# Kernel optimization log

Measured on AMD Instinct MI355X. Metric: run time of the kernel, lower is better.

## Reference

```python
import jax, jax.numpy as jnp
import numpy as np

B, L, D = 4, 16384, 128          # batch, voxels per sample, d_model
DI, DS, DTR, K = 256, 16, 8, 4   # d_inner, d_state, dt_rank, conv kernel
N = B * L
EPS = 1e-5


def setup_inputs() -> dict:
    key = jax.random.key(0)
    ks = jax.random.split(key, 12)
    s = 0.02
    feats = jax.random.normal(ks[0], (N, D), jnp.float32)
    coords_xyz = jax.random.randint(ks[1], (N, 3), 0, 1024, jnp.int32)
    # per-batch Morton permutation + its inverse
    perm = jnp.stack([jax.random.permutation(jax.random.fold_in(ks[2], i), L) for i in range(B)]).astype(jnp.int32)
    inv_perm = jnp.argsort(perm, axis=1).astype(jnp.int32)
    return {
        'feats': feats,
        'pos_w': jax.random.normal(ks[3], (3, D), jnp.float32) * s,
        'pos_b': jnp.zeros((D,), jnp.float32),
        'rms_w': jnp.ones((D,), jnp.float32),
        'in_proj_w': jax.random.normal(ks[4], (D, 2 * DI), jnp.float32) * s,
        'conv_w': jax.random.normal(ks[5], (DI, K), jnp.float32) * s,
        'conv_b': jnp.zeros((DI,), jnp.float32),
        'x_proj_w': jax.random.normal(ks[6], (DI, DTR + 2 * DS), jnp.float32) * s,
        'dt_proj_w': jax.random.normal(ks[7], (DTR, DI), jnp.float32) * s,
        'dt_proj_b': jax.random.normal(ks[8], (DI,), jnp.float32) * 0.1,
        'A_log': jnp.log(jnp.broadcast_to(jnp.arange(1.0, DS + 1.0, dtype=jnp.float32), (DI, DS))),
        'D_param': jnp.ones((DI,), jnp.float32),
        'out_proj_w': jax.random.normal(ks[9], (DI, D), jnp.float32) * s,
        'ln_w': jnp.ones((D,), jnp.float32),
        'ln_b': jnp.zeros((D,), jnp.float32),
        'coords_xyz': coords_xyz,
        'perm': perm,
        'inv_perm': inv_perm,
    }


def _gssm(feats, pos_w, pos_b, rms_w, in_proj_w, conv_w, conv_b, x_proj_w,
          dt_proj_w, dt_proj_b, A_log, D_param, out_proj_w, ln_w, ln_b,
          coords_xyz, perm, inv_perm):
    # positional embedding of voxel coords
    pe = coords_xyz.astype(jnp.float32) @ pos_w + pos_b            # [N, D]
    h = (feats + pe).reshape(B, L, D)
    # gather into Morton order (per-batch fancy index)
    hm = jnp.take_along_axis(h, perm[:, :, None].astype(jnp.int32), axis=1)  # [B, L, D]
    # Mamba block: RMSNorm then mixer (block returns mixer output only)
    x = hm * jax.lax.rsqrt(jnp.mean(hm * hm, axis=-1, keepdims=True) + EPS) * rms_w
    xz = x @ in_proj_w                                             # [B, L, 2*DI]
    xi, z = xz[..., :DI], xz[..., DI:]
    # depthwise causal conv1d, kernel K
    xp = jnp.pad(xi, ((0, 0), (K - 1, 0), (0, 0)))
    xc = conv_b + sum(xp[:, j:j + L, :] * conv_w[:, j] for j in range(K))
    xc = jax.nn.silu(xc)                                           # [B, L, DI]
    dbc = xc @ x_proj_w                                            # [B, L, DTR+2*DS]
    dt, Bm, Cm = dbc[..., :DTR], dbc[..., DTR:DTR + DS], dbc[..., DTR + DS:]
    dt = jax.nn.softplus(dt @ dt_proj_w + dt_proj_b)               # [B, L, DI]
    A = -jnp.exp(A_log)                                            # [DI, DS]

    def step(hst, inp):
        x_t, dt_t, b_t, c_t = inp                                  # [B,DI],[B,DI],[B,DS],[B,DS]
        hst = jnp.exp(dt_t[..., None] * A) * hst + (dt_t * x_t)[..., None] * b_t[:, None, :]
        return hst, jnp.einsum('bds,bs->bd', hst, c_t)

    h0 = jnp.zeros((B, DI, DS), xc.dtype)
    _, ys = jax.lax.scan(step, h0, (xc.transpose(1, 0, 2), dt.transpose(1, 0, 2),
                                    Bm.transpose(1, 0, 2), Cm.transpose(1, 0, 2)))
    y = ys.transpose(1, 0, 2) + xc * D_param                       # [B, L, DI]
    y = y * jax.nn.silu(z)
    out = y @ out_proj_w                                           # [B, L, D]
    # scatter back to original voxel order
    out = jnp.take_along_axis(out, inv_perm[:, :, None].astype(jnp.int32), axis=1).reshape(N, D)
    # post-SSM LayerNorm
    mu = jnp.mean(out, axis=-1, keepdims=True)
    var = jnp.mean((out - mu) ** 2, axis=-1, keepdims=True)
    return (out - mu) * jax.lax.rsqrt(var + EPS) * ln_w + ln_b


def reference(feats, pos_w, pos_b, rms_w, in_proj_w, conv_w, conv_b, x_proj_w,
              dt_proj_w, dt_proj_b, A_log, D_param, out_proj_w, ln_w, ln_b,
              coords_xyz, perm, inv_perm):
    return _gssm(feats, pos_w, pos_b, rms_w, in_proj_w, conv_w, conv_b, x_proj_w,
                 dt_proj_w, dt_proj_b, A_log, D_param, out_proj_w, ln_w, ln_b,
                 coords_xyz, perm, inv_perm)
```

## Files before the change

kernel.cpp:

```cpp
#include <hip/hip_runtime.h>
#include <hip/hip_bf16.h>
#include <math.h>

#define B_   4
#define L_   16384
#define D_   128
#define DI_  256
#define DS_  16
#define DTR_ 8
#define N_   65536
#define NC_  128
#define LC_  128
#define TW_  16
#define TP_  260
#define EPS_ 1e-5f

typedef __hip_bfloat16 bf16;
typedef __attribute__((ext_vector_type(8))) short short8;
typedef __attribute__((ext_vector_type(4))) float f32x4;

__device__ __forceinline__ bool probe_bf16(const void* Dp) {
  return ((const unsigned*)Dp)[0] == 0x3F803F80u;
}
__device__ __forceinline__ float ldin(const void* p, size_t i, bool isb) {
  return isb ? __bfloat162float(((const bf16*)p)[i]) : ((const float*)p)[i];
}
__device__ __forceinline__ float4 ld4(const void* p, size_t i4, bool isb) {
  if (!isb) return ((const float4*)p)[i4];
  const ushort4 v = ((const ushort4*)p)[i4];
  float4 r;
  r.x = __uint_as_float((unsigned)v.x << 16);
  r.y = __uint_as_float((unsigned)v.y << 16);
  r.z = __uint_as_float((unsigned)v.z << 16);
  r.w = __uint_as_float((unsigned)v.w << 16);
  return r;
}
__device__ __forceinline__ void splitbf(float v, ushort& hi, ushort& lo) {
  bf16 h = __float2bfloat16(v);
  float rem = v - __bfloat162float(h);
  bf16 l = __float2bfloat16(rem);
  hi = *(ushort*)&h;
  lo = *(ushort*)&l;
}


__global__ __launch_bounds__(256) void k_xnorm(
    const void* __restrict__ feats, const void* __restrict__ pos_w,
    const void* __restrict__ pos_b, const void* __restrict__ rms_w,
    const int* __restrict__ coords, const int* __restrict__ perm,
    const void* __restrict__ Dprobe,
    ushort* __restrict__ xh, ushort* __restrict__ xl) {
  const bool isb = probe_bf16(Dprobe);
  int wv = threadIdx.x >> 6, lane = threadIdx.x & 63;
  int p = blockIdx.x * 4 + wv;
  int b = p >> 14;
  int srow = b * L_ + perm[p];
  float cx = (float)coords[srow*3+0];
  float cy = (float)coords[srow*3+1];
  float cz = (float)coords[srow*3+2];
  int i0 = lane, i1 = lane + 64;
  float h0 = ldin(feats,(size_t)srow*D_ + i0,isb) + cx*ldin(pos_w,i0,isb) + cy*ldin(pos_w,D_+i0,isb)
           + cz*ldin(pos_w,2*D_+i0,isb) + ldin(pos_b,i0,isb);
  float h1 = ldin(feats,(size_t)srow*D_ + i1,isb) + cx*ldin(pos_w,i1,isb) + cy*ldin(pos_w,D_+i1,isb)
           + cz*ldin(pos_w,2*D_+i1,isb) + ldin(pos_b,i1,isb);
  float ss = h0*h0 + h1*h1;
  #pragma unroll
  for (int off = 32; off; off >>= 1) ss += __shfl_xor(ss, off);
  float r = 1.0f / sqrtf(ss * (1.f/128.f) + EPS_);
  float v0 = h0 * r * ldin(rms_w,i0,isb);
  float v1 = h1 * r * ldin(rms_w,i1,isb);
  ushort a, bq;
  splitbf(v0, a, bq);
  xh[(size_t)p*D_ + i0] = a; xl[(size_t)p*D_ + i0] = bq;
  splitbf(v1, a, bq);
  xh[(size_t)p*D_ + i1] = a; xl[(size_t)p*D_ + i1] = bq;
}

__global__ __launch_bounds__(256) void k_prepw(
    const void* __restrict__ Win, const void* __restrict__ Dprobe,
    ushort* __restrict__ wth, ushort* __restrict__ wtl) {
  const bool isb = probe_bf16(Dprobe);
  int idx = blockIdx.x * 256 + threadIdx.x;
  int k = idx >> 9, n = idx & 511;
  float v = ldin(Win, (size_t)k*512 + n, isb);
  ushort a, b;
  splitbf(v, a, b);
  wth[(size_t)n*128 + k] = a;
  wtl[(size_t)n*128 + k] = b;
}

__global__ __launch_bounds__(256) void k_prepxw(
    const void* __restrict__ xW, const void* __restrict__ Dprobe,
    ushort* __restrict__ wxh, ushort* __restrict__ wxl) {
  const bool isb = probe_bf16(Dprobe);
  int idx = blockIdx.x * 256 + threadIdx.x;
  int q = idx >> 8, c = idx & 255;
  float v = (q < 40) ? ldin(xW, (size_t)c*40 + q, isb) : 0.f;
  ushort a, b;
  splitbf(v, a, b);
  wxh[idx] = a;
  wxl[idx] = b;
}

__global__ __launch_bounds__(256) void k_prepdtw(
    const void* __restrict__ dtW, const void* __restrict__ Dprobe,
    ushort* __restrict__ dtwh, ushort* __restrict__ dtwl) {
  const bool isb = probe_bf16(Dprobe);
  int idx = blockIdx.x * 256 + threadIdx.x;
  int d = idx >> 5, k = idx & 31;
  float v = (k < 8) ? ldin(dtW, (size_t)k*256 + d, isb) : 0.f;
  ushort a, b;
  splitbf(v, a, b);
  dtwh[idx] = a;
  dtwl[idx] = b;
}

__global__ __launch_bounds__(256) void k_inproj(
    const ushort* __restrict__ xh, const ushort* __restrict__ xl,
    const ushort* __restrict__ wth, const ushort* __restrict__ wtl,
    float* __restrict__ xiT, float* __restrict__ zB) {
  __shared__ short Ah[64*136];
  __shared__ short Al[64*136];
  __shared__ short Bh[32*136];
  __shared__ short Bl[32*136];
  int tid = threadIdx.x;
  int T0 = blockIdx.x * 64;
  int lane = tid & 63, w = tid >> 6;
  {
    int k0 = (tid & 15) * 8;
    int m0 = tid >> 4;
    #pragma unroll
    for (int mi = 0; mi < 4; ++mi) {
      int m = m0 + 16*mi;
      *(short8*)&Ah[m*136 + k0] = *(const short8*)&xh[(size_t)(T0+m)*128 + k0];
      *(short8*)&Al[m*136 + k0] = *(const short8*)&xl[(size_t)(T0+m)*128 + k0];
    }
  }
  __syncthreads();
  int mloc = lane & 15, quad = lane >> 4;
  short8 afh[4], afl[4];
  #pragma unroll
  for (int ks = 0; ks < 4; ++ks) {
    int ka = ks*32 + quad*8;
    afh[ks] = *(const short8*)&Ah[(w*16 + mloc)*136 + ka];
    afl[ks] = *(const short8*)&Al[(w*16 + mloc)*136 + ka];
  }
  for (int ct = 0; ct < 16; ++ct) {
    int C0 = ct * 32;
    __syncthreads();
    {
      int k0 = (tid & 15) * 8;
      int n0 = tid >> 4;
      #pragma unroll
      for (int ni = 0; ni < 2; ++ni) {
        int n = n0 + 16*ni;
        *(short8*)&Bh[n*136 + k0] = *(const short8*)&wth[(size_t)(C0+n)*128 + k0];
        *(short8*)&Bl[n*136 + k0] = *(const short8*)&wtl[(size_t)(C0+n)*128 + k0];
      }
    }
    __syncthreads();
    #pragma unroll
    for (int nt = 0; nt < 2; ++nt) {
      f32x4 acc = {0.f, 0.f, 0.f, 0.f};
      #pragma unroll
      for (int ks = 0; ks < 4; ++ks) {
        int kb = ks*32 + quad*8;
        short8 bh = *(const short8*)&Bh[(nt*16 + mloc)*136 + kb];
        short8 bl = *(const short8*)&Bl[(nt*16 + mloc)*136 + kb];
        acc = __builtin_amdgcn_mfma_f32_16x16x32_bf16(afh[ks], bh, acc, 0, 0, 0);
        acc = __builtin_amdgcn_mfma_f32_16x16x32_bf16(afl[ks], bh, acc, 0, 0, 0);
        acc = __builtin_amdgcn_mfma_f32_16x16x32_bf16(afh[ks], bl, acc, 0, 0, 0);
      }
      int col = C0 + nt*16 + mloc;
      int trow = T0 + w*16 + quad*4;
      if (col < 256) {
        *(float4*)&xiT[(size_t)col*N_ + trow] = make_float4(acc[0], acc[1], acc[2], acc[3]);
      } else {
        int zc = col - 256;
        #pragma unroll
        for (int r = 0; r < 4; ++r)
          zB[(size_t)(trow + r)*256 + zc] = acc[r];
      }
    }
  }
}

__global__ __launch_bounds__(256) void k_conv_s(
    const float* __restrict__ xiT, const void* __restrict__ conv_w,
    const void* __restrict__ conv_b, const void* __restrict__ Dprobe,
    float* __restrict__ xcT) {
  const bool isb = probe_bf16(Dprobe);
  int idx = blockIdx.x * 256 + threadIdx.x;
  int c = idx >> 16;
  int t = idx & 65535;
  int l = t & (L_-1);
  const float* row = xiT + (size_t)c * N_;
  float acc = ldin(conv_b, c, isb);
  if (l >= 3) acc += row[t-3] * ldin(conv_w, c*4+0, isb);
  if (l >= 2) acc += row[t-2] * ldin(conv_w, c*4+1, isb);
  if (l >= 1) acc += row[t-1] * ldin(conv_w, c*4+2, isb);
  acc += row[t] * ldin(conv_w, c*4+3, isb);
  xcT[(size_t)c*N_ + t] = acc / (1.f + __expf(-acc));
}

__global__ __launch_bounds__(256) void k_xproj(
    const float* __restrict__ xcT,
    const ushort* __restrict__ wxh, const ushort* __restrict__ wxl,
    const ushort* __restrict__ dtwh, const ushort* __restrict__ dtwl,
    const void* __restrict__ dtb, const void* __restrict__ Dprobe,
    float* __restrict__ dtT, float* __restrict__ BmB, float* __restrict__ CmB) {
  const bool isb = probe_bf16(Dprobe);
  __shared__ float s40[64*52];
  __shared__ float sdtb[256];
  const int tid = threadIdx.x;
  const int lane = tid & 63, w = tid >> 6;
  const int T0 = blockIdx.x * 64;
  const int n15 = lane & 15, quad = lane >> 4;
  sdtb[tid] = ldin(dtb, tid, isb);

  f32x4 acc0 = {0.f,0.f,0.f,0.f}, acc1 = {0.f,0.f,0.f,0.f}, acc2 = {0.f,0.f,0.f,0.f};
  const float* xb = &xcT[(size_t)(quad*8)*N_ + T0 + w*16 + n15];
  #pragma unroll
  for (int ks = 0; ks < 8; ++ks) {
    short8 bh, bl;
    #pragma unroll
    for (int j = 0; j < 8; ++j) {
      ushort h, l;
      splitbf(xb[(size_t)(ks*32 + j)*N_], h, l);
      bh[j] = (short)h; bl[j] = (short)l;
    }
    #pragma unroll
    for (int mt = 0; mt < 3; ++mt) {
      const size_t aoff = (size_t)(mt*16 + n15)*256 + ks*32 + quad*8;
      short8 ah = *(const short8*)&wxh[aoff];
      short8 al = *(const short8*)&wxl[aoff];
      f32x4 a = (mt==0) ? acc0 : (mt==1) ? acc1 : acc2;
      a = __builtin_amdgcn_mfma_f32_16x16x32_bf16(ah, bh, a, 0, 0, 0);
      a = __builtin_amdgcn_mfma_f32_16x16x32_bf16(al, bh, a, 0, 0, 0);
      a = __builtin_amdgcn_mfma_f32_16x16x32_bf16(ah, bl, a, 0, 0, 0);
      if (mt==0) acc0 = a; else if (mt==1) acc1 = a; else acc2 = a;
    }
  }
  {
    const int trow = (w*16 + n15)*52;
    #pragma unroll
    for (int r = 0; r < 4; ++r) {
      s40[trow +      quad*4 + r] = acc0[r];
      s40[trow + 16 + quad*4 + r] = acc1[r];
      s40[trow + 32 + quad*4 + r] = acc2[r];
    }
  }
  __syncthreads();
  {
    int t = tid >> 2, fq = tid & 3;
    float4 bm = *(const float4*)&s40[t*52 + 8  + fq*4];
    float4 cm = *(const float4*)&s40[t*52 + 24 + fq*4];
    *(float4*)&BmB[(size_t)(T0+t)*16 + fq*4] = bm;
    *(float4*)&CmB[(size_t)(T0+t)*16 + fq*4] = cm;
  }
  short8 dh, dl;
  #pragma unroll
  for (int j = 0; j < 8; ++j) {
    ushort h, l;
    splitbf(s40[(w*16 + n15)*52 + quad*8 + j], h, l);
    dh[j] = (short)h; dl[j] = (short)l;
  }
  #pragma unroll
  for (int mt = 0; mt < 16; ++mt) {
    f32x4 a = {0.f,0.f,0.f,0.f};
    const size_t doff = (size_t)(mt*16 + n15)*32 + quad*8;
    short8 ah = *(const short8*)&dtwh[doff];
    short8 al = *(const short8*)&dtwl[doff];
    a = __builtin_amdgcn_mfma_f32_16x16x32_bf16(ah, dh, a, 0, 0, 0);
    a = __builtin_amdgcn_mfma_f32_16x16x32_bf16(al, dh, a, 0, 0, 0);
    a = __builtin_amdgcn_mfma_f32_16x16x32_bf16(ah, dl, a, 0, 0, 0);
    #pragma unroll
    for (int r = 0; r < 4; ++r) {
      int d = mt*16 + quad*4 + r;
      float pre = a[r] + sdtb[d];
      float sp = (pre > 20.f) ? pre : log1pf(__expf(pre));
      dtT[(size_t)d*N_ + T0 + w*16 + n15] = sp;
    }
  }
}

__global__ __launch_bounds__(512, 4) void k_scan1(
    const float* __restrict__ dtT, const float* __restrict__ xcT,
    const float* __restrict__ BmB, const void* __restrict__ A_log,
    const void* __restrict__ Dprobe, float* __restrict__ Pb, float* __restrict__ Sb) {
  const bool isb = probe_bf16(Dprobe);
  __shared__ float sdt[TW_*TP_];
  __shared__ float sxc[TW_*TP_];
  __shared__ float sbm[LC_*16];
  const int tid = threadIdx.x;
  const int blk = blockIdx.x;
  const int b = blk >> 7, ch = blk & 127;
  const int T0 = b * L_ + ch * LC_;
  const int d = tid >> 1, sh = tid & 1, s0 = sh * 8;
  {
    int f = tid * 4;
    *(float4*)&sbm[f] = *(const float4*)&BmB[(size_t)T0*16 + f];
  }
  float Al[8];
  #pragma unroll
  for (int s = 0; s < 8; ++s) Al[s] = -__expf(ldin(A_log, d*16 + s0 + s, isb));
  const float Al0 = (sh == 0) ? Al[0] : -__expf(ldin(A_log, d*16, isb));
  bool fast = true;
  #pragma unroll
  for (int s = 0; s < 8; ++s)
    fast = fast && (fabsf(Al[s] - (Al[0] + (float)s * Al0)) <= 1e-4f * fabsf(Al[s]));
  float h[8];
  #pragma unroll
  for (int s = 0; s < 8; ++s) h[s] = 0.f;
  float sumdt = 0.f;
  float4 vd[2], vx[2];
  #pragma unroll
  for (int q = 0; q < 2; ++q) {
    int idx = q*512 + tid;
    int c2 = idx >> 2, i4 = (idx & 3) * 4;
    size_t off = (size_t)c2*N_ + T0 + i4;
    vd[q] = *(const float4*)&dtT[off];
    vx[q] = *(const float4*)&xcT[off];
  }
  for (int it = 0; it < LC_; it += TW_) {
    __syncthreads();
    #pragma unroll
    for (int q = 0; q < 2; ++q) {
      int idx = q*512 + tid;
      int c2 = idx >> 2, i4 = (idx & 3) * 4;
      sdt[(i4+0)*TP_ + c2] = vd[q].x; sdt[(i4+1)*TP_ + c2] = vd[q].y;
      sdt[(i4+2)*TP_ + c2] = vd[q].z; sdt[(i4+3)*TP_ + c2] = vd[q].w;
      sxc[(i4+0)*TP_ + c2] = vx[q].x; sxc[(i4+1)*TP_ + c2] = vx[q].y;
      sxc[(i4+2)*TP_ + c2] = vx[q].z; sxc[(i4+3)*TP_ + c2] = vx[q].w;
    }
    __syncthreads();
    if (it + TW_ < LC_) {
      #pragma unroll
      for (int q = 0; q < 2; ++q) {
        int idx = q*512 + tid;
        int c2 = idx >> 2, i4 = (idx & 3) * 4;
        size_t off = (size_t)c2*N_ + T0 + it + TW_ + i4;
        vd[q] = *(const float4*)&dtT[off];
        vx[q] = *(const float4*)&xcT[off];
      }
    }
    if (fast) {
      #pragma unroll
      for (int i = 0; i < TW_; ++i) {
        float dtv = sdt[i*TP_ + d];
        float xcv = sxc[i*TP_ + d];
        sumdt += dtv;
        float du = dtv * xcv;
        float e1 = __expf(dtv * Al0);
        float p  = __expf(dtv * Al[0]);
        const float4 b0 = *(const float4*)&sbm[(it+i)*16 + s0];
        const float4 b1 = *(const float4*)&sbm[(it+i)*16 + s0 + 4];
        h[0] = p*h[0] + du*b0.x; p *= e1;
        h[1] = p*h[1] + du*b0.y; p *= e1;
        h[2] = p*h[2] + du*b0.z; p *= e1;
        h[3] = p*h[3] + du*b0.w; p *= e1;
        h[4] = p*h[4] + du*b1.x; p *= e1;
        h[5] = p*h[5] + du*b1.y; p *= e1;
        h[6] = p*h[6] + du*b1.z; p *= e1;
        h[7] = p*h[7] + du*b1.w;
      }
    } else {
      #pragma unroll
      for (int i = 0; i < TW_; ++i) {
        float dtv = sdt[i*TP_ + d];
        float xcv = sxc[i*TP_ + d];
        sumdt += dtv;
        float du = dtv * xcv;
        const float* bmr = &sbm[(it+i)*16 + s0];
        #pragma unroll
        for (int s = 0; s < 8; ++s)
          h[s] = __expf(dtv * Al[s]) * h[s] + du * bmr[s];
      }
    }
  }
  size_t rec = ((size_t)blk*256 + d) * 16 + s0;
  #pragma unroll
  for (int s = 0; s < 8; ++s) {
    Sb[rec + s] = h[s];
    Pb[rec + s] = __expf(Al[s] * sumdt);
  }
}

__global__ __launch_bounds__(256) void k_scan2(
    const float* __restrict__ Pb, const float* __restrict__ Sb, float* __restrict__ Hin) {
  int tid = blockIdx.x * 256 + threadIdx.x;
  int b = tid >> 12, r = tid & 4095;
  float h = 0.f;
  for (int ch = 0; ch < NC_; ++ch) {
    size_t rec = ((size_t)(b*NC_ + ch)) * 4096 + r;
    Hin[rec] = h;
    h = Pb[rec] * h + Sb[rec];
  }
}

__global__ __launch_bounds__(512, 4) void k_scan3(
    const float* __restrict__ dtT, const float* __restrict__ xcT,
    const float* __restrict__ BmB, const float* __restrict__ CmB,
    const void* __restrict__ A_log, const void* __restrict__ Dp,
    const float* __restrict__ Hin, float* __restrict__ zyg) {
  const bool isb = probe_bf16(Dp);
  __shared__ float sdt[TW_*TP_];
  __shared__ float sxc[TW_*TP_];
  __shared__ float sbm[LC_*16];
  __shared__ float scm[LC_*16];
  const int tid = threadIdx.x;
  const int blk = blockIdx.x;
  const int b = blk >> 7, ch = blk & 127;
  const int T0 = b * L_ + ch * LC_;
  const int d = tid >> 1, sh = tid & 1, s0 = sh * 8;
  {
    int f = tid * 4;
    *(float4*)&sbm[f] = *(const float4*)&BmB[(size_t)T0*16 + f];
    *(float4*)&scm[f] = *(const float4*)&CmB[(size_t)T0*16 + f];
  }
  float Al[8];
  #pragma unroll
  for (int s = 0; s < 8; ++s) Al[s] = -__expf(ldin(A_log, d*16 + s0 + s, isb));
  const float Al0 = (sh == 0) ? Al[0] : -__expf(ldin(A_log, d*16, isb));
  bool fast = true;
  #pragma unroll
  for (int s = 0; s < 8; ++s)
    fast = fast && (fabsf(Al[s] - (Al[0] + (float)s * Al0)) <= 1e-4f * fabsf(Al[s]));
  float h[8];
  size_t rec = ((size_t)blk*256 + d) * 16 + s0;
  #pragma unroll
  for (int s = 0; s < 8; ++s) h[s] = Hin[rec + s];
  const float Dv = ldin(Dp, d, isb);
  float4 vd[2], vx[2];
  #pragma unroll
  for (int q = 0; q < 2; ++q) {
    int idx = q*512 + tid;
    int c2 = idx >> 2, i4 = (idx & 3) * 4;
    size_t off = (size_t)c2*N_ + T0 + i4;
    vd[q] = *(const float4*)&dtT[off];
    vx[q] = *(const float4*)&xcT[off];
  }
  for (int it = 0; it < LC_; it += TW_) {
    __syncthreads();
    #pragma unroll
    for (int q = 0; q < 2; ++q) {
      int idx = q*512 + tid;
      int c2 = idx >> 2, i4 = (idx & 3) * 4;
      sdt[(i4+0)*TP_ + c2] = vd[q].x; sdt[(i4+1)*TP_ + c2] = vd[q].y;
      sdt[(i4+2)*TP_ + c2] = vd[q].z; sdt[(i4+3)*TP_ + c2] = vd[q].w;
      sxc[(i4+0)*TP_ + c2] = vx[q].x; sxc[(i4+1)*TP_ + c2] = vx[q].y;
      sxc[(i4+2)*TP_ + c2] = vx[q].z; sxc[(i4+3)*TP_ + c2] = vx[q].w;
    }
    __syncthreads();
    if (it + TW_ < LC_) {
      #pragma unroll
      for (int q = 0; q < 2; ++q) {
        int idx = q*512 + tid;
        int c2 = idx >> 2, i4 = (idx & 3) * 4;
        size_t off = (size_t)c2*N_ + T0 + it + TW_ + i4;
        vd[q] = *(const float4*)&dtT[off];
        vx[q] = *(const float4*)&xcT[off];
      }
    }
    float zv[TW_];
    if (sh == 0) {
      #pragma unroll
      for (int i = 0; i < TW_; ++i) zv[i] = zyg[(size_t)(T0 + it + i)*256 + d];
    }
    #pragma unroll
    for (int i = 0; i < TW_; ++i) {
      float dtv = sdt[i*TP_ + d];
      float xcv = sxc[i*TP_ + d];
      float du = dtv * xcv;
      const float4 b0 = *(const float4*)&sbm[(it+i)*16 + s0];
      const float4 b1 = *(const float4*)&sbm[(it+i)*16 + s0 + 4];
      const float4 c0 = *(const float4*)&scm[(it+i)*16 + s0];
      const float4 c1 = *(const float4*)&scm[(it+i)*16 + s0 + 4];
      float yp = 0.f;
      if (fast) {
        float e1 = __expf(dtv * Al0);
        float p  = __expf(dtv * Al[0]);
        h[0] = p*h[0] + du*b0.x; yp += h[0]*c0.x; p *= e1;
        h[1] = p*h[1] + du*b0.y; yp += h[1]*c0.y; p *= e1;
        h[2] = p*h[2] + du*b0.z; yp += h[2]*c0.z; p *= e1;
        h[3] = p*h[3] + du*b0.w; yp += h[3]*c0.w; p *= e1;
        h[4] = p*h[4] + du*b1.x; yp += h[4]*c1.x; p *= e1;
        h[5] = p*h[5] + du*b1.y; yp += h[5]*c1.y; p *= e1;
        h[6] = p*h[6] + du*b1.z; yp += h[6]*c1.z; p *= e1;
        h[7] = p*h[7] + du*b1.w; yp += h[7]*c1.w;
      } else {
        const float* bmr = &sbm[(it+i)*16 + s0];
        const float* cmr = &scm[(it+i)*16 + s0];
        #pragma unroll
        for (int s = 0; s < 8; ++s) {
          h[s] = __expf(dtv * Al[s]) * h[s] + du * bmr[s];
          yp += h[s] * cmr[s];
        }
      }
      float yt = yp + __shfl_xor(yp, 1);
      if (sh == 0) {
        float yv = yt + xcv * Dv;
        float zvv = zv[i];
        float sil = zvv / (1.f + __expf(-zvv));
        zyg[(size_t)(T0 + it + i)*256 + d] = yv * sil;
      }
    }
  }
}

__global__ __launch_bounds__(256) void k_outproj(
    const float* __restrict__ yg, const void* __restrict__ W2,
    const void* __restrict__ Dprobe, float* __restrict__ outp) {
  const bool isb = probe_bf16(Dprobe);
  __shared__ float As[64*68];
  __shared__ float Bs[64*128];
  int tid = threadIdx.x;
  int T0 = blockIdx.x * 64;
  int tm = tid & 15, tn = tid >> 4;
  float acc[4][8] = {{0.f}};
  for (int kb = 0; kb < 256; kb += 64) {
    {
      int m = tid & 63, kq = tid >> 6;
      #pragma unroll
      for (int r = 0; r < 4; ++r) {
        int k0 = kq*16 + r*4;
        float4 v = *(const float4*)&yg[(size_t)(T0+m)*256 + kb + k0];
        As[(k0+0)*68+m] = v.x; As[(k0+1)*68+m] = v.y;
        As[(k0+2)*68+m] = v.z; As[(k0+3)*68+m] = v.w;
      }
      int n = (tid & 31)*4, kq2 = tid >> 5;
      #pragma unroll
      for (int p = 0; p < 8; ++p) {
        int k = kq2 + p*8;
        float4 w = ld4(W2, ((size_t)(kb+k)*128 + n) >> 2, isb);
        *(float4*)&Bs[k*128 + n] = w;
      }
    }
    __syncthreads();
    #pragma unroll 4
    for (int k = 0; k < 64; ++k) {
      float4 a  = *(const float4*)&As[k*68 + tm*4];
      float4 b0 = *(const float4*)&Bs[k*128 + tn*8];
      float4 b1 = *(const float4*)&Bs[k*128 + tn*8 + 4];
      float am[4] = {a.x, a.y, a.z, a.w};
      float bn[8] = {b0.x, b0.y, b0.z, b0.w, b1.x, b1.y, b1.z, b1.w};
      #pragma unroll
      for (int mi = 0; mi < 4; ++mi)
        #pragma unroll
        for (int ni = 0; ni < 8; ++ni)
          acc[mi][ni] += am[mi] * bn[ni];
    }
    __syncthreads();
  }
  #pragma unroll
  for (int mi = 0; mi < 4; ++mi) {
    size_t m = (size_t)(T0 + tm*4 + mi);
    *(float4*)&outp[m*128 + tn*8]     = make_float4(acc[mi][0], acc[mi][1], acc[mi][2], acc[mi][3]);
    *(float4*)&outp[m*128 + tn*8 + 4] = make_float4(acc[mi][4], acc[mi][5], acc[mi][6], acc[mi][7]);
  }
}

__global__ __launch_bounds__(256) void k_ln(
    const float* __restrict__ outp, const int* __restrict__ perm,
    const void* __restrict__ ln_w, const void* __restrict__ ln_b,
    const void* __restrict__ Dprobe, void* __restrict__ out) {
  const bool isb = probe_bf16(Dprobe);
  int wv = threadIdx.x >> 6, lane = threadIdx.x & 63;
  int p = blockIdx.x * 4 + wv;
  int b = p >> 14;
  int dest = b * L_ + perm[p];
  float v0 = outp[(size_t)p*128 + lane];
  float v1 = outp[(size_t)p*128 + lane + 64];
  float s1 = v0 + v1, s2 = v0*v0 + v1*v1;
  #pragma unroll
  for (int off = 32; off; off >>= 1) {
    s1 += __shfl_xor(s1, off);
    s2 += __shfl_xor(s2, off);
  }
  float mean = s1 * (1.f/128.f);
  float var  = s2 * (1.f/128.f) - mean*mean;
  float r = 1.0f / sqrtf(var + EPS_);
  float o0 = (v0 - mean)*r*ldin(ln_w,lane,isb)    + ldin(ln_b,lane,isb);
  float o1 = (v1 - mean)*r*ldin(ln_w,lane+64,isb) + ldin(ln_b,lane+64,isb);
  if (isb) {
    ((bf16*)out)[(size_t)dest*128 + lane]      = __float2bfloat16(o0);
    ((bf16*)out)[(size_t)dest*128 + lane + 64] = __float2bfloat16(o1);
  } else {
    ((float*)out)[(size_t)dest*128 + lane]      = o0;
    ((float*)out)[(size_t)dest*128 + lane + 64] = o1;
  }
}

extern "C" void kernel_launch(void* const* d_in, const int* in_sizes, int n_in,
                              void* d_out, int out_size, void* d_ws, size_t ws_size,
                              hipStream_t stream) {
  const void* feats    = d_in[0];
  const void* pos_w    = d_in[1];
  const void* pos_b    = d_in[2];
  const void* rms_w    = d_in[3];
  const void* in_proj  = d_in[4];
  const void* conv_w   = d_in[5];
  const void* conv_b   = d_in[6];
  const void* x_proj   = d_in[7];
  const void* dt_projw = d_in[8];
  const void* dt_projb = d_in[9];
  const void* A_log    = d_in[10];
  const void* D_param  = d_in[11];
  const void* out_proj = d_in[12];
  const void* ln_w     = d_in[13];
  const void* ln_b     = d_in[14];
  const int*  coords   = (const int*)d_in[15];
  const int*  perm     = (const int*)d_in[16];

  float* ws = (float*)d_ws;
  const size_t NN = (size_t)N_;
  ushort* xh  = (ushort*)ws;
  ushort* xl  = (ushort*)(ws + 64*NN);
  ushort* wth = (ushort*)(ws + 640*NN);
  ushort* wtl = (ushort*)(ws + 641*NN);
  ushort* wxh  = (ushort*)ws;
  ushort* wxl  = ((ushort*)ws) + 12288;
  ushort* dtwh = ((ushort*)ws) + 24576;
  ushort* dtwl = ((ushort*)ws) + 32768;
  float* Pb   = ws;
  float* Sb   = ws + 32*NN;
  float* Hin  = ws + 64*NN;
  float* BmB  = ws + 96*NN;
  float* CmB  = ws + 112*NN;
  float* xiT  = ws + 128*NN;
  float* dtT  = ws + 128*NN;
  float* outp = ws + 128*NN;
  float* zB   = ws + 384*NN;
  float* yg   = zB;
  float* xcT  = ws + 640*NN;

  k_prepw<<<256, 256, 0, stream>>>(in_proj, D_param, wth, wtl);
  k_xnorm<<<N_/4, 256, 0, stream>>>(feats, pos_w, pos_b, rms_w, coords, perm, D_param, xh, xl);
  k_inproj<<<N_/64, 256, 0, stream>>>(xh, xl, wth, wtl, xiT, zB);
  k_prepxw<<<48, 256, 0, stream>>>(x_proj, D_param, wxh, wxl);
  k_prepdtw<<<32, 256, 0, stream>>>(dt_projw, D_param, dtwh, dtwl);
  k_conv_s<<<(DI_*N_)/256, 256, 0, stream>>>(xiT, conv_w, conv_b, D_param, xcT);
  k_xproj<<<N_/64, 256, 0, stream>>>(xcT, wxh, wxl, dtwh, dtwl, dt_projb, D_param, dtT, BmB, CmB);
  k_scan1<<<B_*NC_, 512, 0, stream>>>(dtT, xcT, BmB, A_log, D_param, Pb, Sb);
  k_scan2<<<64, 256, 0, stream>>>(Pb, Sb, Hin);
  k_scan3<<<B_*NC_, 512, 0, stream>>>(dtT, xcT, BmB, CmB, A_log, D_param, Hin, zB);
  k_outproj<<<N_/64, 256, 0, stream>>>(yg, out_proj, D_param, outp);
  k_ln<<<N_/4, 256, 0, stream>>>(outp, perm, ln_w, ln_b, D_param, d_out);
}
```

Baseline: 543.0 us.

## Store z/y-gated buffer channel-major and give each scan thread all 16 states

The z half of in_proj is now written channel-major ([DI][N]) with float4 stores instead of scattered token-major stores. The scan3 kernel uses 256 threads per block, each owning one channel and all 16 states, so it no longer needs the lane-pair shuffle reduction. It reads and writes z/y as float4 along the token axis. out_proj now loads its A tile directly from the channel-major layout without an in-shared transpose. The trade is fewer threads per block and more registers per thread in the scan, which lowers parallelism inside the sequential recurrence.

```diff
diff --git a/kernel.cpp b/kernel.cpp
--- a/kernel.cpp
+++ b/kernel.cpp
@@ -118,7 +118,7 @@
 __global__ __launch_bounds__(256) void k_inproj(
     const ushort* __restrict__ xh, const ushort* __restrict__ xl,
     const ushort* __restrict__ wth, const ushort* __restrict__ wtl,
-    float* __restrict__ xiT, float* __restrict__ zB) {
+    float* __restrict__ xiT, float* __restrict__ zT) {
   __shared__ short Ah[64*136];
   __shared__ short Al[64*136];
   __shared__ short Bh[32*136];
@@ -176,10 +176,7 @@
       if (col < 256) {
         *(float4*)&xiT[(size_t)col*N_ + trow] = make_float4(acc[0], acc[1], acc[2], acc[3]);
       } else {
-        int zc = col - 256;
-        #pragma unroll
-        for (int r = 0; r < 4; ++r)
-          zB[(size_t)(trow + r)*256 + zc] = acc[r];
+        *(float4*)&zT[(size_t)(col-256)*N_ + trow] = make_float4(acc[0], acc[1], acc[2], acc[3]);
       }
     }
   }
@@ -398,11 +395,11 @@
   }
 }
 
-__global__ __launch_bounds__(512, 4) void k_scan3(
+__global__ __launch_bounds__(256) void k_scan3(
     const float* __restrict__ dtT, const float* __restrict__ xcT,
     const float* __restrict__ BmB, const float* __restrict__ CmB,
     const void* __restrict__ A_log, const void* __restrict__ Dp,
-    const float* __restrict__ Hin, float* __restrict__ zyg) {
+    const float* __restrict__ Hin, float* __restrict__ zyT) {
   const bool isb = probe_bf16(Dp);
   __shared__ float sdt[TW_*TP_];
   __shared__ float sxc[TW_*TP_];
@@ -412,99 +409,131 @@
   const int blk = blockIdx.x;
   const int b = blk >> 7, ch = blk & 127;
   const int T0 = b * L_ + ch * LC_;
-  const int d = tid >> 1, sh = tid & 1, s0 = sh * 8;
-  {
-    int f = tid * 4;
+  const int d = tid;
+  #pragma unroll
+  for (int p = 0; p < 2; ++p) {
+    int f = (p*256 + tid) * 4;
     *(float4*)&sbm[f] = *(const float4*)&BmB[(size_t)T0*16 + f];
     *(float4*)&scm[f] = *(const float4*)&CmB[(size_t)T0*16 + f];
   }
-  float Al[8];
-  #pragma unroll
-  for (int s = 0; s < 8; ++s) Al[s] = -__expf(ldin(A_log, d*16 + s0 + s, isb));
-  const float Al0 = (sh == 0) ? Al[0] : -__expf(ldin(A_log, d*16, isb));
+  float Al[16];
+  #pragma unroll
+  for (int s = 0; s < 16; ++s) Al[s] = -__expf(ldin(A_log, d*16 + s, isb));
   bool fast = true;
   #pragma unroll
-  for (int s = 0; s < 8; ++s)
-    fast = fast && (fabsf(Al[s] - (Al[0] + (float)s * Al0)) <= 1e-4f * fabsf(Al[s]));
-  float h[8];
-  size_t rec = ((size_t)blk*256 + d) * 16 + s0;
-  #pragma unroll
-  for (int s = 0; s < 8; ++s) h[s] = Hin[rec + s];
+  for (int s = 1; s < 16; ++s)
+    fast = fast && (fabsf(Al[s] - (float)(s+1) * Al[0]) <= 1e-4f * fabsf(Al[s]));
+  float h[16];
+  size_t rec = ((size_t)blk*256 + d) * 16;
+  #pragma unroll
+  for (int s = 0; s < 16; ++s) h[s] = Hin[rec + s];
   const float Dv = ldin(Dp, d, isb);
   float4 vd[2], vx[2];
   #pragma unroll
   for (int q = 0; q < 2; ++q) {
-    int idx = q*512 + tid;
-    int c2 = idx >> 2, i4 = (idx & 3) * 4;
+    int idx = q*256 + tid;
+    int c2 = idx >> 1, i4 = (idx & 1) * 8;
     size_t off = (size_t)c2*N_ + T0 + i4;
     vd[q] = *(const float4*)&dtT[off];
     vx[q] = *(const float4*)&xcT[off];
   }
+  float4 vd2[2], vx2[2];
+  #pragma unroll
+  for (int q = 0; q < 2; ++q) {
+    int idx = q*256 + tid;
+    int c2 = idx >> 1, i4 = (idx & 1) * 8;
+    size_t off = (size_t)c2*N_ + T0 + i4 + 4;
+    vd2[q] = *(const float4*)&dtT[off];
+    vx2[q] = *(const float4*)&xcT[off];
+  }
   for (int it = 0; it < LC_; it += TW_) {
     __syncthreads();
     #pragma unroll
     for (int q = 0; q < 2; ++q) {
-      int idx = q*512 + tid;
-      int c2 = idx >> 2, i4 = (idx & 3) * 4;
+      int idx = q*256 + tid;
+      int c2 = idx >> 1, i4 = (idx & 1) * 8;
       sdt[(i4+0)*TP_ + c2] = vd[q].x; sdt[(i4+1)*TP_ + c2] = vd[q].y;
       sdt[(i4+2)*TP_ + c2] = vd[q].z; sdt[(i4+3)*TP_ + c2] = vd[q].w;
       sxc[(i4+0)*TP_ + c2] = vx[q].x; sxc[(i4+1)*TP_ + c2] = vx[q].y;
       sxc[(i4+2)*TP_ + c2] = vx[q].z; sxc[(i4+3)*TP_ + c2] = vx[q].w;
+      sdt[(i4+4)*TP_ + c2] = vd2[q].x; sdt[(i4+5)*TP_ + c2] = vd2[q].y;
+      sdt[(i4+6)*TP_ + c2] = vd2[q].z; sdt[(i4+7)*TP_ + c2] = vd2[q].w;
+      sxc[(i4+4)*TP_ + c2] = vx2[q].x; sxc[(i4+5)*TP_ + c2] = vx2[q].y;
+      sxc[(i4+6)*TP_ + c2] = vx2[q].z; sxc[(i4+7)*TP_ + c2] = vx2[q].w;
     }
     __syncthreads();
     if (it + TW_ < LC_) {
       #pragma unroll
       for (int q = 0; q < 2; ++q) {
-        int idx = q*512 + tid;
-        int c2 = idx >> 2, i4 = (idx & 3) * 4;
+        int idx = q*256 + tid;
+        int c2 = idx >> 1, i4 = (idx & 1) * 8;
         size_t off = (size_t)c2*N_ + T0 + it + TW_ + i4;
         vd[q] = *(const float4*)&dtT[off];
         vx[q] = *(const float4*)&xcT[off];
-      }
-    }
-    float zv[TW_];
-    if (sh == 0) {
-      #pragma unroll
-      for (int i = 0; i < TW_; ++i) zv[i] = zyg[(size_t)(T0 + it + i)*256 + d];
-    }
+        vd2[q] = *(const float4*)&dtT[off + 4];
+        vx2[q] = *(const float4*)&xcT[off + 4];
+      }
+    }
+    float4 zq[4];
+    #pragma unroll
+    for (int j = 0; j < 4; ++j)
+      zq[j] = *(const float4*)&zyT[(size_t)d*N_ + T0 + it + j*4];
+    const float zf[16] = {zq[0].x, zq[0].y, zq[0].z, zq[0].w,
+                          zq[1].x, zq[1].y, zq[1].z, zq[1].w,
+                          zq[2].x, zq[2].y, zq[2].z, zq[2].w,
+                          zq[3].x, zq[3].y, zq[3].z, zq[3].w};
+    float ov[16];
     #pragma unroll
     for (int i = 0; i < TW_; ++i) {
       float dtv = sdt[i*TP_ + d];
       float xcv = sxc[i*TP_ + d];
       float du = dtv * xcv;
-      const float4 b0 = *(const float4*)&sbm[(it+i)*16 + s0];
-      const float4 b1 = *(const float4*)&sbm[(it+i)*16 + s0 + 4];
-      const float4 c0 = *(const float4*)&scm[(it+i)*16 + s0];
-      const float4 c1 = *(const float4*)&scm[(it+i)*16 + s0 + 4];
+      const float4 b0 = *(const float4*)&sbm[(it+i)*16];
+      const float4 b1 = *(const float4*)&sbm[(it+i)*16 + 4];
+      const float4 b2 = *(const float4*)&sbm[(it+i)*16 + 8];
+      const float4 b3 = *(const float4*)&sbm[(it+i)*16 + 12];
+      const float4 c0 = *(const float4*)&scm[(it+i)*16];
+      const float4 c1 = *(const float4*)&scm[(it+i)*16 + 4];
+      const float4 c2 = *(const float4*)&scm[(it+i)*16 + 8];
+      const float4 c3 = *(const float4*)&scm[(it+i)*16 + 12];
       float yp = 0.f;
       if (fast) {
-        float e1 = __expf(dtv * Al0);
-        float p  = __expf(dtv * Al[0]);
-        h[0] = p*h[0] + du*b0.x; yp += h[0]*c0.x; p *= e1;
-        h[1] = p*h[1] + du*b0.y; yp += h[1]*c0.y; p *= e1;
-        h[2] = p*h[2] + du*b0.z; yp += h[2]*c0.z; p *= e1;
-        h[3] = p*h[3] + du*b0.w; yp += h[3]*c0.w; p *= e1;
-        h[4] = p*h[4] + du*b1.x; yp += h[4]*c1.x; p *= e1;
-        h[5] = p*h[5] + du*b1.y; yp += h[5]*c1.y; p *= e1;
-        h[6] = p*h[6] + du*b1.z; yp += h[6]*c1.z; p *= e1;
-        h[7] = p*h[7] + du*b1.w; yp += h[7]*c1.w;
+        float e1 = __expf(dtv * Al[0]);
+        float p = e1;
+        h[0]  = p*h[0]  + du*b0.x; yp += h[0] *c0.x; p *= e1;
+        h[1]  = p*h[1]  + du*b0.y; yp += h[1] *c0.y; p *= e1;
+        h[2]  = p*h[2]  + du*b0.z; yp += h[2] *c0.z; p *= e1;
+        h[3]  = p*h[3]  + du*b0.w; yp += h[3] *c0.w; p *= e1;
+        h[4]  = p*h[4]  + du*b1.x; yp += h[4] *c1.x; p *= e1;
+        h[5]  = p*h[5]  + du*b1.y; yp += h[5] *c1.y; p *= e1;
+        h[6]  = p*h[6]  + du*b1.z; yp += h[6] *c1.z; p *= e1;
+        h[7]  = p*h[7]  + du*b1.w; yp += h[7] *c1.w; p *= e1;
+        h[8]  = p*h[8]  + du*b2.x; yp += h[8] *c2.x; p *= e1;
+        h[9]  = p*h[9]  + du*b2.y; yp += h[9] *c2.y; p *= e1;
+        h[10] = p*h[10] + du*b2.z; yp += h[10]*c2.z; p *= e1;
+        h[11] = p*h[11] + du*b2.w; yp += h[11]*c2.w; p *= e1;
+        h[12] = p*h[12] + du*b3.x; yp += h[12]*c3.x; p *= e1;
+        h[13] = p*h[13] + du*b3.y; yp += h[13]*c3.y; p *= e1;
+        h[14] = p*h[14] + du*b3.z; yp += h[14]*c3.z; p *= e1;
+        h[15] = p*h[15] + du*b3.w; yp += h[15]*c3.w;
       } else {
-        const float* bmr = &sbm[(it+i)*16 + s0];
-        const float* cmr = &scm[(it+i)*16 + s0];
+        const float* bmr = &sbm[(it+i)*16];
+        const float* cmr = &scm[(it+i)*16];
         #pragma unroll
-        for (int s = 0; s < 8; ++s) {
+        for (int s = 0; s < 16; ++s) {
           h[s] = __expf(dtv * Al[s]) * h[s] + du * bmr[s];
           yp += h[s] * cmr[s];
         }
       }
-      float yt = yp + __shfl_xor(yp, 1);
-      if (sh == 0) {
-        float yv = yt + xcv * Dv;
-        float zvv = zv[i];
-        float sil = zvv / (1.f + __expf(-zvv));
-        zyg[(size_t)(T0 + it + i)*256 + d] = yv * sil;
-      }
-    }
+      float yv = yp + xcv * Dv;
+      float zvv = zf[i];
+      float sil = zvv / (1.f + __expf(-zvv));
+      ov[i] = yv * sil;
+    }
+    #pragma unroll
+    for (int j = 0; j < 4; ++j)
+      *(float4*)&zyT[(size_t)d*N_ + T0 + it + j*4] =
+          make_float4(ov[j*4], ov[j*4+1], ov[j*4+2], ov[j*4+3]);
   }
 }
 
@@ -520,20 +549,19 @@
   float acc[4][8] = {{0.f}};
   for (int kb = 0; kb < 256; kb += 64) {
     {
-      int m = tid & 63, kq = tid >> 6;
+      int k = tid >> 2, mq = (tid & 3) * 16;
+      const float* src = &yg[(size_t)(kb + k)*N_ + T0 + mq];
       #pragma unroll
       for (int r = 0; r < 4; ++r) {
-        int k0 = kq*16 + r*4;
-        float4 v = *(const float4*)&yg[(size_t)(T0+m)*256 + kb + k0];
-        As[(k0+0)*68+m] = v.x; As[(k0+1)*68+m] = v.y;
-        As[(k0+2)*68+m] = v.z; As[(k0+3)*68+m] = v.w;
+        float4 v = *(const float4*)&src[r*4];
+        *(float4*)&As[k*68 + mq + r*4] = v;
       }
       int n = (tid & 31)*4, kq2 = tid >> 5;
       #pragma unroll
       for (int p = 0; p < 8; ++p) {
-        int k = kq2 + p*8;
-        float4 w = ld4(W2, ((size_t)(kb+k)*128 + n) >> 2, isb);
-        *(float4*)&Bs[k*128 + n] = w;
+        int k2 = kq2 + p*8;
+        float4 w = ld4(W2, ((size_t)(kb+k2)*128 + n) >> 2, isb);
+        *(float4*)&Bs[k2*128 + n] = w;
       }
     }
     __syncthreads();
@@ -630,20 +658,20 @@
   float* xiT  = ws + 128*NN;
   float* dtT  = ws + 128*NN;
   float* outp = ws + 128*NN;
-  float* zB   = ws + 384*NN;
-  float* yg   = zB;
+  float* zT   = ws + 384*NN;
+  float* yg   = zT;
   float* xcT  = ws + 640*NN;
 
   k_prepw<<<256, 256, 0, stream>>>(in_proj, D_param, wth, wtl);
   k_xnorm<<<N_/4, 256, 0, stream>>>(feats, pos_w, pos_b, rms_w, coords, perm, D_param, xh, xl);
-  k_inproj<<<N_/64, 256, 0, stream>>>(xh, xl, wth, wtl, xiT, zB);
+  k_inproj<<<N_/64, 256, 0, stream>>>(xh, xl, wth, wtl, xiT, zT);
   k_prepxw<<<48, 256, 0, stream>>>(x_proj, D_param, wxh, wxl);
   k_prepdtw<<<32, 256, 0, stream>>>(dt_projw, D_param, dtwh, dtwl);
   k_conv_s<<<(DI_*N_)/256, 256, 0, stream>>>(xiT, conv_w, conv_b, D_param, xcT);
   k_xproj<<<N_/64, 256, 0, stream>>>(xcT, wxh, wxl, dtwh, dtwl, dt_projb, D_param, dtT, BmB, CmB);
   k_scan1<<<B_*NC_, 512, 0, stream>>>(dtT, xcT, BmB, A_log, D_param, Pb, Sb);
   k_scan2<<<64, 256, 0, stream>>>(Pb, Sb, Hin);
-  k_scan3<<<B_*NC_, 512, 0, stream>>>(dtT, xcT, BmB, CmB, A_log, D_param, Hin, zB);
+  k_scan3<<<B_*NC_, 256, 0, stream>>>(dtT, xcT, BmB, CmB, A_log, D_param, Hin, zT);
   k_outproj<<<N_/64, 256, 0, stream>>>(yg, out_proj, D_param, outp);
   k_ln<<<N_/4, 256, 0, stream>>>(outp, perm, ln_w, ln_b, D_param, d_out);
 }
```

Result: no change. 542.9 us (-0.0%).
